# Optimization experiments

Measured on AMD Instinct MI355X. Metric: run time of the kernel, lower is better.

## Reference

```python
import jax, jax.numpy as jnp
import numpy as np

B, T, FEATS, HEAD = 2, 2048, 2048, 16
DIM_HEAD = FEATS // HEAD
EPS = float(jnp.finfo(jnp.float32).eps)  # torch nn.RMSNorm default eps=None -> dtype eps


def _rms_norm(u, g):
    # u: [..., d]; torch RMSNorm: u / sqrt(mean(u^2) + eps) * g
    return u * jax.lax.rsqrt(jnp.mean(u * u, axis=-1, keepdims=True) + EPS) * g


def setup_inputs() -> dict:
    key = jax.random.key(0)
    kx, kw = jax.random.split(key)
    x = jax.random.normal(kx, (B, T, FEATS), dtype=jnp.float32)
    W = jax.random.normal(kw, (FEATS, FEATS), dtype=jnp.float32) / np.sqrt(FEATS)
    g1 = jnp.ones((DIM_HEAD,), dtype=jnp.float32)
    g2 = jnp.ones((DIM_HEAD,), dtype=jnp.float32)
    g3 = jnp.ones((DIM_HEAD,), dtype=jnp.float32)
    return {"x": x, "W": W, "g1": g1, "g2": g2, "g3": g3}


def reference(x, W, g1, g2, g3):
    Bb, Tt, C = x.shape
    sqrt_d = jnp.asarray(DIM_HEAD ** 0.5, dtype=x.dtype)
    # tied QKV projection: torch Linear -> x @ W.T ; then split heads -> [B,H,T,D]
    w = (x @ W.T).reshape(Bb, Tt, HEAD, DIM_HEAD).transpose(0, 2, 1, 3)
    q = _rms_norm(w, g1)
    k = _rms_norm(w, g2)
    v = _rms_norm(w, g3)
    att = jnp.einsum("bhid,bhjd->bhij", q, k) / sqrt_d  # [B,H,T,T]
    # symmetric row + column softmax
    score = jax.nn.softmax(att, axis=-1) + jax.nn.softmax(att, axis=-2)
    y = jnp.einsum("bhij,bhjd->bihd", score, v).reshape(Bb, Tt, C)
    # F.linear(y, W.t()) == y @ W  (tied-weight reprojection)
    return y @ W
```

## Files before the change

### kernel.cpp

```cpp
#include <hip/hip_runtime.h>
#include <stdint.h>

#define T_SEQ 2048
#define B_SZ 2
#define N_HEAD 16
#define D_HEAD 128
#define C_DIM 2048
#define M_ROWS (B_SZ*T_SEQ)
#define N_BH (B_SZ*N_HEAD)

typedef _Float16 f16;
typedef f16 f16x8 __attribute__((ext_vector_type(8)));
typedef f16 f16x4 __attribute__((ext_vector_type(4)));
typedef float f32x4 __attribute__((ext_vector_type(4)));

#define MFMA_F16(a,b,c) __builtin_amdgcn_mfma_f32_16x16x32_f16(a,b,c,0,0,0)

#define BAR_LGKM() do { asm volatile("s_waitcnt lgkmcnt(0)" ::: "memory"); \
                        __builtin_amdgcn_s_barrier(); } while (0)
#define BAR_ALL()  do { asm volatile("s_waitcnt vmcnt(0) lgkmcnt(0)" ::: "memory"); \
                        __builtin_amdgcn_s_barrier(); } while (0)

__device__ __forceinline__ void gl_lds16(const void* g, void* l) {
  __builtin_amdgcn_global_load_lds(
      (const __attribute__((address_space(1))) unsigned int*)g,
      (__attribute__((address_space(3))) unsigned int*)l, 16, 0, 0);
}

__global__ void k_prep_w(const float* __restrict__ W, f16* __restrict__ Wb,
                         f16* __restrict__ Wtb) {
  __shared__ float tile[64][65];
  const int bx = blockIdx.x * 64;
  const int by = blockIdx.y * 64;
  const int t = threadIdx.x;
  const int tc = t & 63, tr4 = t >> 6;
  for (int rr = tr4; rr < 64; rr += 4) {
    float v = W[(size_t)(by + rr) * C_DIM + bx + tc];
    tile[rr][tc] = v;
    Wb[(size_t)(by + rr) * C_DIM + bx + tc] = (f16)v;
  }
  __syncthreads();
  for (int rr = tr4; rr < 64; rr += 4) {
    Wtb[(size_t)(bx + rr) * C_DIM + by + tc] = (f16)tile[tc][rr];
  }
}

__global__ void k_prep_x(const float* __restrict__ x, f16* __restrict__ xb) {
  int i = blockIdx.x * blockDim.x + threadIdx.x;
  const int stride = gridDim.x * blockDim.x;
  const int n4 = (M_ROWS * C_DIM) / 4;
  for (; i < n4; i += stride) {
    f32x4 v = ((const f32x4*)x)[i];
    f16x4 o; o[0]=(f16)v[0]; o[1]=(f16)v[1]; o[2]=(f16)v[2]; o[3]=(f16)v[3];
    ((f16x4*)xb)[i] = o;
  }
}

template<typename OT>
__global__ __launch_bounds__(256, 2)
void k_gemm_bt(const f16* __restrict__ A, const f16* __restrict__ Bm,
               OT* __restrict__ C, int Nd, int Kd) {
  __shared__ __align__(16) f16 As[2][128 * 64];
  __shared__ __align__(16) f16 Bs[2][128 * 64];
  const int tid = threadIdx.x;
  const int lane = tid & 63, wid = tid >> 6;
  const int lr = lane & 15, lkg = lane >> 4;
  const int wr = wid >> 1, wc = wid & 1;
  const int tm = blockIdx.y * 128, tn = blockIdx.x * 128;

  f32x4 acc[4][4];
#pragma unroll
  for (int i = 0; i < 4; ++i)
#pragma unroll
    for (int j = 0; j < 4; ++j) acc[i][j] = (f32x4){0.f, 0.f, 0.f, 0.f};

  const int nkt = Kd >> 6;

  auto stage = [&](int buf, int kt) {
    const int k0 = kt << 6;
    for (int s = 0; s < 4; ++s) {
      const int r0 = (wid * 4 + s) * 8;
      const int r = r0 + (lane >> 3);
      const int lg = ((lane & 7) ^ (r & 7)) << 3;
      gl_lds16(A + (size_t)(tm + r) * Kd + k0 + lg, &As[buf][r0 * 64]);
      gl_lds16(Bm + (size_t)(tn + r) * Kd + k0 + lg, &Bs[buf][r0 * 64]);
    }
  };

  stage(0, 0);
  int cur = 0;
  for (int kt = 0; kt < nkt; ++kt) {
    __syncthreads();
    if (kt + 1 < nkt) stage(cur ^ 1, kt + 1);
#pragma unroll
    for (int kk = 0; kk < 2; ++kk) {
      f16x8 a[4], b[4];
#pragma unroll
      for (int i = 0; i < 4; ++i) {
        const int ra = wr * 64 + i * 16 + lr;
        const int ga = ((kk * 4 + lkg) ^ (ra & 7)) << 3;
        a[i] = *(const f16x8*)&As[cur][ra * 64 + ga];
        const int rb = wc * 64 + i * 16 + lr;
        const int gb = ((kk * 4 + lkg) ^ (rb & 7)) << 3;
        b[i] = *(const f16x8*)&Bs[cur][rb * 64 + gb];
      }
#pragma unroll
      for (int i = 0; i < 4; ++i)
#pragma unroll
        for (int j = 0; j < 4; ++j) acc[i][j] = MFMA_F16(a[i], b[j], acc[i][j]);
    }
    cur ^= 1;
  }
#pragma unroll
  for (int i = 0; i < 4; ++i) {
    const int row0 = tm + wr * 64 + i * 16 + lkg * 4;
#pragma unroll
    for (int j = 0; j < 4; ++j) {
      const int col = tn + wc * 64 + j * 16 + lr;
#pragma unroll
      for (int r = 0; r < 4; ++r)
        C[(size_t)(row0 + r) * Nd + col] = (OT)acc[i][j][r];
    }
  }
}

__global__ __launch_bounds__(256, 4)
void k_rms(const f16* __restrict__ wb, const float* __restrict__ g1,
           const float* __restrict__ g2, f16* __restrict__ nb,
           f16* __restrict__ mb) {
  const int tid = threadIdx.x, lane = tid & 63, wid = tid >> 6;
  const int lr = lane & 15, grp = lane >> 4;
  float gs[8];
#pragma unroll
  for (int e = 0; e < 8; ++e)
    gs[e] = g1[lr * 8 + e] * g2[lr * 8 + e] * 0.08838834764831843f;
  const int R = blockIdx.x * 16 + wid * 4 + grp;
  const f16x8 w8 = *(const f16x8*)&wb[(size_t)R * 128 + lr * 8];
  float f[8];
  float ss = 0.f;
#pragma unroll
  for (int e = 0; e < 8; ++e) { f[e] = (float)w8[e]; ss += f[e] * f[e]; }
  ss += __shfl_xor(ss, 1); ss += __shfl_xor(ss, 2);
  ss += __shfl_xor(ss, 4); ss += __shfl_xor(ss, 8);
  const float scale = rsqrtf(ss * (1.f / 128.f) + 1.1920928955078125e-07f);
  const int hh = R & (N_HEAD - 1);
  const int bt = R >> 4;
  const int b = bt >> 11;
  const int t = bt & (T_SEQ - 1);
  const size_t dst = ((size_t)((b * N_HEAD + hh) * T_SEQ + t)) * 128 + lr * 8;
  f16x8 n8, m8;
#pragma unroll
  for (int e = 0; e < 8; ++e) {
    float nf = f[e] * scale;
    n8[e] = (f16)nf;
    m8[e] = (f16)(nf * gs[e]);
  }
  *(f16x8*)&nb[dst] = n8;
  *(f16x8*)&mb[dst] = m8;
}

__global__ void k_tn(const f16* __restrict__ nin, f16* __restrict__ nT) {
  __shared__ __align__(16) f16 tile[64][72];
  const int t = threadIdx.x;
  const int c = t & 7, r4 = t >> 3;
  const int bh = blockIdx.z, t0 = blockIdx.x * 64, d0 = blockIdx.y * 64;
  const f16* src = nin + ((size_t)bh * T_SEQ + t0) * 128 + d0;
  for (int rr = r4; rr < 64; rr += 32)
    *(f16x8*)&tile[rr][c * 8] = *(const f16x8*)&src[(size_t)rr * 128 + c * 8];
  __syncthreads();
  f16* dst = nT + ((size_t)bh * 128 + d0) * T_SEQ + t0;
  for (int rr = r4; rr < 64; rr += 32) {
    f16x8 v;
#pragma unroll
    for (int e = 0; e < 8; ++e) v[e] = tile[c * 8 + e][rr];
    *(f16x8*)&dst[(size_t)rr * T_SEQ + c * 8] = v;
  }
}

__global__ __launch_bounds__(256, 2)
void k_stats(const f16* __restrict__ mIn, const f16* __restrict__ nIn,
             float* __restrict__ alpha) {
  __shared__ __align__(16) f16 Ns[2][128 * 128];
  __shared__ float red[256];
  const int tid = threadIdx.x, lane = tid & 63, wid = tid >> 6;
  const int lr = lane & 15, lkg = lane >> 4;
  const int wr = wid >> 1, wc = wid & 1;
  const int lin = blockIdx.x + (blockIdx.y << 4);
  const int swz = ((lin & 7) << 6) + (lin >> 3);
  const int it = swz & 15, bh = swz >> 4;
  const f16* mp = mIn + (size_t)bh * T_SEQ * 128;
  const f16* np = nIn + (size_t)bh * T_SEQ * 128;

  f16x8 msr[4][4];
#pragma unroll
  for (int i = 0; i < 4; ++i)
#pragma unroll
    for (int kk = 0; kk < 4; ++kk)
      msr[i][kk] = *(const f16x8*)&mp[(size_t)(it * 128 + wr * 64 + i * 16 + lr) * 128 +
                                      (kk * 4 + lkg) * 8];

  auto stageN = [&](int buf, int jt) {
#pragma unroll
    for (int s = 0; s < 8; ++s) {
      const int r0 = (wid * 8 + s) * 4;
      const int r = r0 + (lane >> 4);
      const int lg = ((lane & 15) ^ (r & 7)) << 3;
      gl_lds16(np + (size_t)(jt * 128 + r) * 128 + lg, &Ns[buf][r0 * 128]);
    }
  };

  float srun[16];
#pragma unroll
  for (int q = 0; q < 16; ++q) srun[q] = 0.f;

  stageN(0, 0);
  BAR_ALL();
  int cur = 0;
  for (int jt = 0; jt < 16; ++jt) {
    if (jt < 15) stageN(cur ^ 1, jt + 1);
    f32x4 acc[4][4];
#pragma unroll
    for (int i = 0; i < 4; ++i)
#pragma unroll
      for (int j = 0; j < 4; ++j) acc[i][j] = (f32x4){0.f, 0.f, 0.f, 0.f};
#pragma unroll
    for (int kk = 0; kk < 4; ++kk) {
      f16x8 b[4];
#pragma unroll
      for (int j = 0; j < 4; ++j) {
        const int rb = wc * 64 + j * 16 + lr;
        const int gb = ((kk * 4 + lkg) ^ (rb & 7)) << 3;
        b[j] = *(const f16x8*)&Ns[cur][rb * 128 + gb];
      }
#pragma unroll
      for (int i = 0; i < 4; ++i)
#pragma unroll
        for (int j = 0; j < 4; ++j)
          acc[i][j] = MFMA_F16(msr[i][kk], b[j], acc[i][j]);
    }
#pragma unroll
    for (int i = 0; i < 4; ++i)
#pragma unroll
      for (int r = 0; r < 4; ++r) {
        float s = __expf(acc[i][0][r]) + __expf(acc[i][1][r]) +
                  __expf(acc[i][2][r]) + __expf(acc[i][3][r]);
        srun[i * 4 + r] += s;
      }
    BAR_ALL();
    cur ^= 1;
  }
#pragma unroll
  for (int q = 0; q < 16; ++q) {
    float v = srun[q];
    v += __shfl_xor(v, 1); v += __shfl_xor(v, 2);
    v += __shfl_xor(v, 4); v += __shfl_xor(v, 8);
    srun[q] = v;
  }
  if (lr == 0) {
#pragma unroll
    for (int q = 0; q < 16; ++q) {
      const int row = wr * 64 + (q >> 2) * 16 + lkg * 4 + (q & 3);
      red[row * 2 + wc] = srun[q];
    }
  }
  __syncthreads();
  if (tid < 128) {
    const float s = red[tid * 2] + red[tid * 2 + 1];
    alpha[(size_t)bh * T_SEQ + it * 128 + tid] = 1.f / s;
  }
}

__global__ __launch_bounds__(256, 2)
void k_apply(const f16* __restrict__ mIn, const f16* __restrict__ nIn,
             const f16* __restrict__ nTIn, const float* __restrict__ alpha,
             const float* __restrict__ g3, f16* __restrict__ yb) {
  __shared__ __align__(16) f16 Ns[2][64 * 128];
  __shared__ __align__(16) f16 Nts[2][128 * 64];
  __shared__ __align__(16) f16 Ps[128 * 64];
  const int tid = threadIdx.x, lane = tid & 63, wid = tid >> 6;
  const int lr = lane & 15, lkg = lane >> 4;
  const int wj = wid >> 1;
  const int wi = wid & 1;
  const int lin = blockIdx.x + (blockIdx.y << 4);
  const int swz = ((lin & 7) << 6) + (lin >> 3);
  const int it = swz & 15, bh = swz >> 4;
  const int b = bh >> 4, hh = bh & 15;
  const f16* mp = mIn + (size_t)bh * T_SEQ * 128;
  const f16* np = nIn + (size_t)bh * T_SEQ * 128;
  const f16* ntp = nTIn + (size_t)bh * 128 * T_SEQ;
  const float* al = alpha + (size_t)bh * T_SEQ;

  f16x8 msr[4][4];
#pragma unroll
  for (int ii = 0; ii < 4; ++ii)
#pragma unroll
    for (int kk = 0; kk < 4; ++kk)
      msr[ii][kk] = *(const f16x8*)&mp[(size_t)(it * 128 + wi * 64 + ii * 16 + lr) * 128 +
                                       (kk * 4 + lkg) * 8];

  auto stageN = [&](int buf, int jt) {
#pragma unroll
    for (int s = 0; s < 4; ++s) {
      const int r0 = (wid * 4 + s) * 4;
      const int r = r0 + (lane >> 4);
      const int lg = ((lane & 15) ^ (r & 7)) << 3;
      gl_lds16(np + (size_t)(jt * 64 + r) * 128 + lg, &Ns[buf][r0 * 128]);
    }
  };
  auto stageNT = [&](int buf, int jt) {
#pragma unroll
    for (int s = 0; s < 4; ++s) {
      const int r0 = (wid * 4 + s) * 8;
      const int r = r0 + (lane >> 3);
      const int lg = ((lane & 7) ^ (r & 7)) << 3;
      gl_lds16(ntp + (size_t)r * T_SEQ + jt * 64 + lg, &Nts[buf][r0 * 64]);
    }
  };

  float ai[4];
#pragma unroll
  for (int ii = 0; ii < 4; ++ii) ai[ii] = al[it * 128 + wi * 64 + ii * 16 + lr];

  f32x4 yacc[4][4];
#pragma unroll
  for (int i = 0; i < 4; ++i)
#pragma unroll
    for (int j = 0; j < 4; ++j) yacc[i][j] = (f32x4){0.f, 0.f, 0.f, 0.f};

  stageN(0, 0);
  stageNT(0, 0);
  BAR_ALL();
  int cur = 0;
  for (int jt = 0; jt < 32; ++jt) {
    float aj[8];
#pragma unroll
    for (int jj = 0; jj < 2; ++jj)
#pragma unroll
      for (int r = 0; r < 4; ++r)
        aj[jj * 4 + r] = al[jt * 64 + wj * 32 + jj * 16 + lkg * 4 + r];
    if (jt < 31) { stageN(cur ^ 1, jt + 1); stageNT(cur ^ 1, jt + 1); }

    f32x4 acc[2][4];
#pragma unroll
    for (int i = 0; i < 2; ++i)
#pragma unroll
      for (int j = 0; j < 4; ++j) acc[i][j] = (f32x4){0.f, 0.f, 0.f, 0.f};
#pragma unroll
    for (int kk = 0; kk < 4; ++kk) {
      f16x8 a[2];
#pragma unroll
      for (int jj = 0; jj < 2; ++jj) {
        const int jrow = wj * 32 + jj * 16 + lr;
        a[jj] = *(const f16x8*)&Ns[cur][jrow * 128 + (((kk * 4 + lkg) ^ (jrow & 7)) << 3)];
      }
#pragma unroll
      for (int jj = 0; jj < 2; ++jj)
#pragma unroll
        for (int ii = 0; ii < 4; ++ii)
          acc[jj][ii] = MFMA_F16(a[jj], msr[ii][kk], acc[jj][ii]);
    }

#pragma unroll
    for (int jj = 0; jj < 2; ++jj)
#pragma unroll
      for (int ii = 0; ii < 4; ++ii) {
        f16x4 o;
#pragma unroll
        for (int r = 0; r < 4; ++r) {
          const float p = __expf(acc[jj][ii][r]) * (ai[ii] + aj[jj * 4 + r]);
          o[r] = (f16)p;
        }
        const int il = wi * 64 + ii * 16 + lr;
        const int jl = wj * 32 + jj * 16 + lkg * 4;
        *(f16x4*)&Ps[il * 64 + (((jl >> 3) ^ (il & 7)) << 3) + (jl & 7)] = o;
      }
    BAR_LGKM();

#pragma unroll
    for (int kk = 0; kk < 2; ++kk) {
      f16x8 a[4], bfr[4];
#pragma unroll
      for (int dd = 0; dd < 4; ++dd) {
        const int drow = wj * 64 + dd * 16 + lr;
        a[dd] = *(const f16x8*)&Nts[cur][drow * 64 + (((kk * 4 + lkg) ^ (drow & 7)) << 3)];
      }
#pragma unroll
      for (int ii = 0; ii < 4; ++ii) {
        const int irow = wi * 64 + ii * 16 + lr;
        bfr[ii] = *(const f16x8*)&Ps[irow * 64 + (((kk * 4 + lkg) ^ (irow & 7)) << 3)];
      }
#pragma unroll
      for (int dd = 0; dd < 4; ++dd)
#pragma unroll
        for (int ii = 0; ii < 4; ++ii)
          yacc[dd][ii] = MFMA_F16(a[dd], bfr[ii], yacc[dd][ii]);
    }
    BAR_ALL();
    cur ^= 1;
  }

#pragma unroll
  for (int dd = 0; dd < 4; ++dd) {
    const int d0 = wj * 64 + dd * 16 + lkg * 4;
    float g3v[4];
#pragma unroll
    for (int r = 0; r < 4; ++r) g3v[r] = g3[d0 + r];
#pragma unroll
    for (int ii = 0; ii < 4; ++ii) {
      const int icol = wi * 64 + ii * 16 + lr;
      const size_t base =
          ((size_t)(b * T_SEQ + it * 128 + icol)) * C_DIM + hh * 128 + d0;
      f16x4 o;
#pragma unroll
      for (int r = 0; r < 4; ++r) o[r] = (f16)(yacc[dd][ii][r] * g3v[r]);
      *(f16x4*)&yb[base] = o;
    }
  }
}

extern "C" void kernel_launch(void* const* d_in, const int* in_sizes, int n_in,
                              void* d_out, int out_size, void* d_ws,
                              size_t ws_size, hipStream_t stream) {
  const float* x = (const float*)d_in[0];
  const float* W = (const float*)d_in[1];
  const float* g1 = (const float*)d_in[2];
  const float* g2 = (const float*)d_in[3];
  const float* g3 = (const float*)d_in[4];
  float* out = (float*)d_out;
  char* ws = (char*)d_ws;

  f16* xb   = (f16*)(ws);
  f16* Wb   = (f16*)(ws + 16777216);
  f16* Wtb  = (f16*)(ws + 25165824);
  f16* wb   = (f16*)(ws + 33554432);
  f16* nb   = (f16*)(ws + 50331648);
  f16* mb   = (f16*)(ws + 67108864);
  f16* nT   = (f16*)(ws + 83886080);
  f16* yb   = (f16*)(ws + 100663296);
  float* alpha = (float*)(ws + 117440512);

  k_prep_w<<<dim3(32, 32), 256, 0, stream>>>(W, Wb, Wtb);
  k_prep_x<<<dim3(2048), 256, 0, stream>>>(x, xb);
  k_gemm_bt<f16><<<dim3(16, 32), 256, 0, stream>>>(xb, Wb, wb, C_DIM, C_DIM);
  k_rms<<<dim3(4096), 256, 0, stream>>>(wb, g1, g2, nb, mb);
  k_tn<<<dim3(32, 2, 32), 256, 0, stream>>>(nb, nT);
  k_stats<<<dim3(16, 32), 256, 0, stream>>>(mb, nb, alpha);
  k_apply<<<dim3(16, 32), 256, 0, stream>>>(mb, nb, nT, alpha, g3, yb);
  k_gemm_bt<float><<<dim3(16, 32), 256, 0, stream>>>(yb, Wtb, out, C_DIM, C_DIM);
}
```

Baseline: 242.9 us.

## Fuse QKV GEMM with RMSNorm and transpose; use exp2 and MFMA priority hints

Replaces the separate QKV GEMM, RMS-norm and transpose kernels with one GEMM whose 128-wide N tile matches a head. The epilogue stages C in LDS, computes per-row RMS scales, and writes the normalized, scaled and transposed outputs directly. This removes the intermediate wb buffer round trip and two launches. The softmax scale now folds log2(e) into mb, so the kernels can call exp2f instead of __expf. s_setprio is raised around the MFMA blocks in the stats and apply kernels. The fused kernel uses about 69 KB of LDS, which limits occupancy.

```diff
diff --git a/kernel.cpp b/kernel.cpp
--- a/kernel.cpp
+++ b/kernel.cpp
@@ -26,6 +26,9 @@
       (const __attribute__((address_space(1))) unsigned int*)g,
       (__attribute__((address_space(3))) unsigned int*)l, 16, 0, 0);
 }
+
+#define MB_SCALE 0.12752924444069595f
+#define RMS_EPS  1.1920928955078125e-07f
 
 __global__ void k_prep_w(const float* __restrict__ W, f16* __restrict__ Wb,
                          f16* __restrict__ Wtb) {
@@ -124,56 +127,123 @@
   }
 }
 
-__global__ __launch_bounds__(256, 4)
-void k_rms(const f16* __restrict__ wb, const float* __restrict__ g1,
-           const float* __restrict__ g2, f16* __restrict__ nb,
-           f16* __restrict__ mb) {
-  const int tid = threadIdx.x, lane = tid & 63, wid = tid >> 6;
-  const int lr = lane & 15, grp = lane >> 4;
-  float gs[8];
-#pragma unroll
-  for (int e = 0; e < 8; ++e)
-    gs[e] = g1[lr * 8 + e] * g2[lr * 8 + e] * 0.08838834764831843f;
-  const int R = blockIdx.x * 16 + wid * 4 + grp;
-  const f16x8 w8 = *(const f16x8*)&wb[(size_t)R * 128 + lr * 8];
-  float f[8];
+__global__ __launch_bounds__(256, 2)
+void k_gemm_qkv(const f16* __restrict__ A, const f16* __restrict__ Bm,
+                const float* __restrict__ g1, const float* __restrict__ g2,
+                f16* __restrict__ nb, f16* __restrict__ mb,
+                f16* __restrict__ nT) {
+  __shared__ __align__(16) char smem[70656];
+  f16 (*As)[128 * 64] = (f16(*)[128 * 64])smem;
+  f16 (*Bs)[128 * 64] = (f16(*)[128 * 64])(smem + 32768);
+  f16* Cs = (f16*)smem;
+  float* sc = (float*)(smem + 69632);
+
+  const int tid = threadIdx.x;
+  const int lane = tid & 63, wid = tid >> 6;
+  const int lr = lane & 15, lkg = lane >> 4;
+  const int wr = wid >> 1, wc = wid & 1;
+  const int tm = blockIdx.y * 128;
+  const int hh = blockIdx.x;
+  const int tn = hh * 128;
+
+  f32x4 acc[4][4];
+#pragma unroll
+  for (int i = 0; i < 4; ++i)
+#pragma unroll
+    for (int j = 0; j < 4; ++j) acc[i][j] = (f32x4){0.f, 0.f, 0.f, 0.f};
+
+  auto stage = [&](int buf, int kt) {
+    const int k0 = kt << 6;
+    for (int s = 0; s < 4; ++s) {
+      const int r0 = (wid * 4 + s) * 8;
+      const int r = r0 + (lane >> 3);
+      const int lg = ((lane & 7) ^ (r & 7)) << 3;
+      gl_lds16(A + (size_t)(tm + r) * C_DIM + k0 + lg, &As[buf][r0 * 64]);
+      gl_lds16(Bm + (size_t)(tn + r) * C_DIM + k0 + lg, &Bs[buf][r0 * 64]);
+    }
+  };
+
+  stage(0, 0);
+  int cur = 0;
+  for (int kt = 0; kt < 32; ++kt) {
+    __syncthreads();
+    if (kt + 1 < 32) stage(cur ^ 1, kt + 1);
+#pragma unroll
+    for (int kk = 0; kk < 2; ++kk) {
+      f16x8 a[4], b[4];
+#pragma unroll
+      for (int i = 0; i < 4; ++i) {
+        const int ra = wr * 64 + i * 16 + lr;
+        const int ga = ((kk * 4 + lkg) ^ (ra & 7)) << 3;
+        a[i] = *(const f16x8*)&As[cur][ra * 64 + ga];
+        const int rb = wc * 64 + i * 16 + lr;
+        const int gb = ((kk * 4 + lkg) ^ (rb & 7)) << 3;
+        b[i] = *(const f16x8*)&Bs[cur][rb * 64 + gb];
+      }
+#pragma unroll
+      for (int i = 0; i < 4; ++i)
+#pragma unroll
+        for (int j = 0; j < 4; ++j) acc[i][j] = MFMA_F16(a[i], b[j], acc[i][j]);
+    }
+    cur ^= 1;
+  }
+  __syncthreads();
+
+#pragma unroll
+  for (int i = 0; i < 4; ++i)
+#pragma unroll
+    for (int j = 0; j < 4; ++j)
+#pragma unroll
+      for (int r = 0; r < 4; ++r)
+        Cs[(wr * 64 + i * 16 + lkg * 4 + r) * 136 + wc * 64 + j * 16 + lr] =
+            (f16)acc[i][j][r];
+  __syncthreads();
+
+  const int row = tid >> 1, dh = tid & 1;
+  f16x8 v[8];
   float ss = 0.f;
 #pragma unroll
-  for (int e = 0; e < 8; ++e) { f[e] = (float)w8[e]; ss += f[e] * f[e]; }
-  ss += __shfl_xor(ss, 1); ss += __shfl_xor(ss, 2);
-  ss += __shfl_xor(ss, 4); ss += __shfl_xor(ss, 8);
-  const float scale = rsqrtf(ss * (1.f / 128.f) + 1.1920928955078125e-07f);
-  const int hh = R & (N_HEAD - 1);
-  const int bt = R >> 4;
-  const int b = bt >> 11;
-  const int t = bt & (T_SEQ - 1);
-  const size_t dst = ((size_t)((b * N_HEAD + hh) * T_SEQ + t)) * 128 + lr * 8;
-  f16x8 n8, m8;
-#pragma unroll
-  for (int e = 0; e < 8; ++e) {
-    float nf = f[e] * scale;
-    n8[e] = (f16)nf;
-    m8[e] = (f16)(nf * gs[e]);
-  }
-  *(f16x8*)&nb[dst] = n8;
-  *(f16x8*)&mb[dst] = m8;
-}
-
-__global__ void k_tn(const f16* __restrict__ nin, f16* __restrict__ nT) {
-  __shared__ __align__(16) f16 tile[64][72];
-  const int t = threadIdx.x;
-  const int c = t & 7, r4 = t >> 3;
-  const int bh = blockIdx.z, t0 = blockIdx.x * 64, d0 = blockIdx.y * 64;
-  const f16* src = nin + ((size_t)bh * T_SEQ + t0) * 128 + d0;
-  for (int rr = r4; rr < 64; rr += 32)
-    *(f16x8*)&tile[rr][c * 8] = *(const f16x8*)&src[(size_t)rr * 128 + c * 8];
+  for (int c = 0; c < 8; ++c) {
+    v[c] = *(const f16x8*)&Cs[row * 136 + dh * 64 + c * 8];
+#pragma unroll
+    for (int e = 0; e < 8; ++e) { float f = (float)v[c][e]; ss += f * f; }
+  }
+  ss += __shfl_xor(ss, 1);
+  const float scale = rsqrtf(ss * (1.f / 128.f) + RMS_EPS);
+  if (dh == 0) sc[row] = scale;
+
+  const int grow = tm + row;
+  const int b = grow >> 11, ts = grow & (T_SEQ - 1);
+  const size_t nbase =
+      ((size_t)((b * N_HEAD + hh) * T_SEQ + ts)) * 128 + dh * 64;
+#pragma unroll
+  for (int c = 0; c < 8; ++c) {
+    const int d0 = dh * 64 + c * 8;
+    f16x8 n8, m8;
+#pragma unroll
+    for (int e = 0; e < 8; ++e) {
+      const float nf = (float)v[c][e] * scale;
+      n8[e] = (f16)nf;
+      m8[e] = (f16)(nf * g1[d0 + e] * g2[d0 + e] * MB_SCALE);
+    }
+    *(f16x8*)&nb[nbase + c * 8] = n8;
+    *(f16x8*)&mb[nbase + c * 8] = m8;
+  }
   __syncthreads();
-  f16* dst = nT + ((size_t)bh * 128 + d0) * T_SEQ + t0;
-  for (int rr = r4; rr < 64; rr += 32) {
-    f16x8 v;
-#pragma unroll
-    for (int e = 0; e < 8; ++e) v[e] = tile[c * 8 + e][rr];
-    *(f16x8*)&dst[(size_t)rr * T_SEQ + c * 8] = v;
+
+  const int dcol = tid >> 1, th = tid & 1;
+  const size_t tbase =
+      ((size_t)((b * N_HEAD + hh) * 128 + dcol)) * T_SEQ + (tm & (T_SEQ - 1)) +
+      th * 64;
+#pragma unroll
+  for (int rr = 0; rr < 8; ++rr) {
+    f16x8 o;
+#pragma unroll
+    for (int e = 0; e < 8; ++e) {
+      const int trow = th * 64 + rr * 8 + e;
+      o[e] = (f16)((float)Cs[trow * 136 + dcol] * sc[trow]);
+    }
+    *(f16x8*)&nT[tbase + rr * 8] = o;
   }
 }
 
@@ -223,6 +293,7 @@
     for (int i = 0; i < 4; ++i)
 #pragma unroll
       for (int j = 0; j < 4; ++j) acc[i][j] = (f32x4){0.f, 0.f, 0.f, 0.f};
+    __builtin_amdgcn_s_setprio(1);
 #pragma unroll
     for (int kk = 0; kk < 4; ++kk) {
       f16x8 b[4];
@@ -238,12 +309,13 @@
         for (int j = 0; j < 4; ++j)
           acc[i][j] = MFMA_F16(msr[i][kk], b[j], acc[i][j]);
     }
+    __builtin_amdgcn_s_setprio(0);
 #pragma unroll
     for (int i = 0; i < 4; ++i)
 #pragma unroll
       for (int r = 0; r < 4; ++r) {
-        float s = __expf(acc[i][0][r]) + __expf(acc[i][1][r]) +
-                  __expf(acc[i][2][r]) + __expf(acc[i][3][r]);
+        float s = exp2f(acc[i][0][r]) + exp2f(acc[i][1][r]) +
+                  exp2f(acc[i][2][r]) + exp2f(acc[i][3][r]);
         srun[i * 4 + r] += s;
       }
     BAR_ALL();
@@ -345,6 +417,7 @@
     for (int i = 0; i < 2; ++i)
 #pragma unroll
       for (int j = 0; j < 4; ++j) acc[i][j] = (f32x4){0.f, 0.f, 0.f, 0.f};
+    __builtin_amdgcn_s_setprio(1);
 #pragma unroll
     for (int kk = 0; kk < 4; ++kk) {
       f16x8 a[2];
@@ -359,6 +432,7 @@
         for (int ii = 0; ii < 4; ++ii)
           acc[jj][ii] = MFMA_F16(a[jj], msr[ii][kk], acc[jj][ii]);
     }
+    __builtin_amdgcn_s_setprio(0);
 
 #pragma unroll
     for (int jj = 0; jj < 2; ++jj)
@@ -367,7 +441,7 @@
         f16x4 o;
 #pragma unroll
         for (int r = 0; r < 4; ++r) {
-          const float p = __expf(acc[jj][ii][r]) * (ai[ii] + aj[jj * 4 + r]);
+          const float p = exp2f(acc[jj][ii][r]) * (ai[ii] + aj[jj * 4 + r]);
           o[r] = (f16)p;
         }
         const int il = wi * 64 + ii * 16 + lr;
@@ -376,6 +450,7 @@
       }
     BAR_LGKM();
 
+    __builtin_amdgcn_s_setprio(1);
 #pragma unroll
     for (int kk = 0; kk < 2; ++kk) {
       f16x8 a[4], bfr[4];
@@ -395,6 +470,7 @@
         for (int ii = 0; ii < 4; ++ii)
           yacc[dd][ii] = MFMA_F16(a[dd], bfr[ii], yacc[dd][ii]);
     }
+    __builtin_amdgcn_s_setprio(0);
     BAR_ALL();
     cur ^= 1;
   }
@@ -432,7 +508,6 @@
   f16* xb   = (f16*)(ws);
   f16* Wb   = (f16*)(ws + 16777216);
   f16* Wtb  = (f16*)(ws + 25165824);
-  f16* wb   = (f16*)(ws + 33554432);
   f16* nb   = (f16*)(ws + 50331648);
   f16* mb   = (f16*)(ws + 67108864);
   f16* nT   = (f16*)(ws + 83886080);
@@ -441,9 +516,7 @@
 
   k_prep_w<<<dim3(32, 32), 256, 0, stream>>>(W, Wb, Wtb);
   k_prep_x<<<dim3(2048), 256, 0, stream>>>(x, xb);
-  k_gemm_bt<f16><<<dim3(16, 32), 256, 0, stream>>>(xb, Wb, wb, C_DIM, C_DIM);
-  k_rms<<<dim3(4096), 256, 0, stream>>>(wb, g1, g2, nb, mb);
-  k_tn<<<dim3(32, 2, 32), 256, 0, stream>>>(nb, nT);
+  k_gemm_qkv<<<dim3(16, 32), 256, 0, stream>>>(xb, Wb, g1, g2, nb, mb, nT);
   k_stats<<<dim3(16, 32), 256, 0, stream>>>(mb, nb, alpha);
   k_apply<<<dim3(16, 32), 256, 0, stream>>>(mb, nb, nT, alpha, g3, yb);
   k_gemm_bt<float><<<dim3(16, 32), 256, 0, stream>>>(yb, Wtb, out, C_DIM, C_DIM);
```

Measured after the change: 259.3 us. +6.7%, slower.
